# Performance work log

Hardware: AMD Instinct MI355X
Metric: run time of the kernel (lower is better)

## Reference

```python
import jax, jax.numpy as jnp
import numpy as np
from jax import lax

T_H = 16
B = 16384
GW, GH = 3, 13          # masks are (B, grid_w, grid_h, enc) so permute -> (B, enc, 13, 3)
ENC = 64                # encoder_size
IN_EMB = 32             # input_embedding_size
DYN = 32                # dyn_embedding_size
SCD = 64                # soc_conv_depth
C31 = 16                # conv_3x1_depth
SOC_EMB = ((GH - 4 + 1) // 2) * C31  # 80
N_CELLS = B * GW * GH
N_NBRS = (N_CELLS + 1) // 2  # every other grid cell occupied -> 319488
NEG_SLOPE = 0.1


def leaky(x):
    return jnp.where(x >= 0, x, NEG_SLOPE * x)


def lstm_last_hidden(x, Wih, Whh, bih, bhh):
    """x: (T, N, in). PyTorch gate order i,f,g,o. Returns final h: (N, H)."""
    H = Whh.shape[1]
    N = x.shape[1]
    b = bih + bhh
    def step(carry, xt):
        h, c = carry
        gates = xt @ Wih.T + h @ Whh.T + b  # (N, 4H)
        i, f, g, o = jnp.split(gates, 4, axis=-1)
        c = jax.nn.sigmoid(f) * c + jax.nn.sigmoid(i) * jnp.tanh(g)
        h = jax.nn.sigmoid(o) * jnp.tanh(c)
        return (h, c), None
    h0 = jnp.zeros((N, H), x.dtype)
    (h, _), _ = lax.scan(step, (h0, h0), x)
    return h


def conv2d(x, W, b, ):
    y = lax.conv_general_dilated(x, W, window_strides=(1, 1), padding='VALID',
                                 dimension_numbers=('NCHW', 'OIHW', 'NCHW'))
    return y + b[None, :, None, None]


def setup_inputs() -> dict:
    key = jax.random.key(0)
    ks = jax.random.split(key, 10)
    hist = jax.random.normal(ks[0], (T_H, B, 2), jnp.float32)
    nbrs = jax.random.normal(ks[1], (T_H, N_NBRS, 2), jnp.float32)
    # Occupancy: every other cell; masked_scatter_ fills a full 64-vector per occupied cell.
    flat_occ = (jnp.arange(N_CELLS) % 2) == 0
    masks = jnp.broadcast_to(flat_occ.reshape(B, GW, GH, 1), (B, GW, GH, ENC))
    s = 0.05
    W_ip = jax.random.normal(ks[2], (IN_EMB, 2), jnp.float32) * s
    b_ip = jnp.zeros((IN_EMB,), jnp.float32)
    Wih = jax.random.normal(ks[3], (4 * ENC, IN_EMB), jnp.float32) * s
    Whh = jax.random.normal(ks[4], (4 * ENC, ENC), jnp.float32) * s
    bih = jnp.zeros((4 * ENC,), jnp.float32)
    bhh = jnp.zeros((4 * ENC,), jnp.float32)
    W_dyn = jax.random.normal(ks[5], (DYN, ENC), jnp.float32) * s
    b_dyn = jnp.zeros((DYN,), jnp.float32)
    W_sc = jax.random.normal(ks[6], (SCD, ENC, 3, 3), jnp.float32) * s
    b_sc = jnp.zeros((SCD,), jnp.float32)
    W_c31 = jax.random.normal(ks[7], (C31, SCD, 3, 1), jnp.float32) * s
    b_c31 = jnp.zeros((C31,), jnp.float32)
    return dict(hist=hist, nbrs=nbrs, masks=masks, W_ip=W_ip, b_ip=b_ip,
                Wih=Wih, Whh=Whh, bih=bih, bhh=bhh, W_dyn=W_dyn, b_dyn=b_dyn,
                W_sc=W_sc, b_sc=b_sc, W_c31=W_c31, b_c31=b_c31)


def reference(hist, nbrs, masks, W_ip, b_ip, Wih, Whh, bih, bhh,
              W_dyn, b_dyn, W_sc, b_sc, W_c31, b_c31):
    # 1. ego dynamics
    hist_emb = leaky(hist @ W_ip.T + b_ip)                 # (T, B, 32)
    hist_enc = lstm_last_hidden(hist_emb, Wih, Whh, bih, bhh)  # (B, 64)
    hist_enc = leaky(hist_enc @ W_dyn.T + b_dyn)           # (B, 32)
    # 2. neighbour encodings
    nbrs_emb = leaky(nbrs @ W_ip.T + b_ip)                 # (T, N, 32)
    nbrs_enc = lstm_last_hidden(nbrs_emb, Wih, Whh, bih, bhh)  # (N, 64)
    # 3. masked_scatter_: scatter nbrs_enc rows into occupied grid cells in row-major order
    occ = masks[:, :, :, 0].reshape(-1)                    # (B*GW*GH,) bool
    idx = jnp.cumsum(occ.astype(jnp.int32)) - 1            # nbr index per occupied cell
    gathered = nbrs_enc[jnp.clip(idx, 0, None)]            # (B*GW*GH, 64)
    soc = jnp.where(occ[:, None], gathered, 0.0).reshape(B, GW, GH, ENC)
    # 4. permute(0,3,2,1) -> (B, enc, GH, GW)
    soc = soc.transpose(0, 3, 2, 1)
    soc = leaky(conv2d(soc, W_sc, b_sc))                   # (B, 64, 11, 1)
    soc = leaky(conv2d(soc, W_c31, b_c31))                 # (B, 16, 9, 1)
    # 5. MaxPool2d((2,1), padding=(1,0)) with -inf padding
    soc = lax.reduce_window(soc, -jnp.inf, lax.max,
                            window_dimensions=(1, 1, 2, 1), window_strides=(1, 1, 2, 1),
                            padding=((0, 0), (0, 0), (1, 1), (0, 0)))  # (B,16,5,1)
    soc = soc.reshape(-1, SOC_EMB)                         # (B, 80)
    return jnp.concatenate([soc, hist_enc], axis=1)        # (B, 112)
```

## Files before the change

kernel.cpp:

```cpp
#include <hip/hip_runtime.h>
#include <cstdint>

#define T_H 16
#define B_SZ 16384
#define NN 319488

#define EROWP 40
#define HROWP 72
#define W1R 72
#define NB_NBR 4992
#define NB_HIST 256
#define CHUNK 8192
#define O1STR 704
#define LOG2E 1.4426950408889634f
#define M2L   2.8853900817779268f

typedef __attribute__((ext_vector_type(8))) _Float16 f16x8;
typedef __attribute__((ext_vector_type(4))) float f32x4;

__device__ __forceinline__ float lrelu(float x) { return fmaxf(x, 0.1f * x); }

__device__ __forceinline__ f16x8 cvt8(const float* __restrict__ p, float sc) {
    float4 a = ((const float4*)p)[0];
    float4 b = ((const float4*)p)[1];
    f16x8 r;
    r[0] = (_Float16)(a.x * sc); r[1] = (_Float16)(a.y * sc);
    r[2] = (_Float16)(a.z * sc); r[3] = (_Float16)(a.w * sc);
    r[4] = (_Float16)(b.x * sc); r[5] = (_Float16)(b.y * sc);
    r[6] = (_Float16)(b.z * sc); r[7] = (_Float16)(b.w * sc);
    return r;
}

__global__ __launch_bounds__(256, 3) void lstm_coop(
    const float* __restrict__ hist, const float* __restrict__ nbrs,
    const float* __restrict__ Wip, const float* __restrict__ bip,
    const float* __restrict__ Wih, const float* __restrict__ Whh,
    const float* __restrict__ bsum,
    const float* __restrict__ Wdyn, const float* __restrict__ bdyn,
    _Float16* __restrict__ ench, float* __restrict__ out)
{
    __shared__ alignas(16) _Float16 eb[2][64 * EROWP];
    __shared__ alignas(16) _Float16 hb[2][64 * HROWP];

    const int tid = threadIdx.x;
    const int wid = tid >> 6;
    const int lane = tid & 63;
    const int col = lane & 15;
    const int quad = lane >> 4;

    const bool ishist = (blockIdx.x >= NB_NBR);
    const int seq0 = (ishist ? (blockIdx.x - NB_NBR) : blockIdx.x) * 64;
    const int N = ishist ? B_SZ : NN;
    const float2* __restrict__ xp = (const float2*)(ishist ? hist : nbrs);

    f16x8 Bv[4][3];
#pragma unroll
    for (int gt = 0; gt < 4; gt++) {
        const float sc = (gt == 2) ? M2L : -LOG2E;
        const int row = gt * 64 + wid * 16 + col;
        Bv[gt][0] = cvt8(Wih + row * 32 + quad * 8,      sc);
        Bv[gt][1] = cvt8(Whh + row * 64 + quad * 8,      sc);
        Bv[gt][2] = cvt8(Whh + row * 64 + 32 + quad * 8, sc);
    }
    float bg4[4];
#pragma unroll
    for (int gt = 0; gt < 4; gt++) bg4[gt] = bsum[gt * 64 + wid * 16 + col];

    float wipx[8], wipy[8], bipv[8];
#pragma unroll
    for (int u = 0; u < 8; u++) {
        int j = quad * 8 + u;
        wipx[u] = Wip[2 * j]; wipy[u] = Wip[2 * j + 1]; bipv[u] = bip[j];
    }

    float c[16];
#pragma unroll
    for (int q = 0; q < 16; q++) c[q] = 0.0f;

    {
        float2 xv = xp[seq0 + wid * 16 + col];
        f16x8 E;
#pragma unroll
        for (int u = 0; u < 8; u++)
            E[u] = (_Float16)lrelu(fmaf(xv.x, wipx[u], fmaf(xv.y, wipy[u], bipv[u])));
        *(f16x8*)&eb[0][(wid * 16 + col) * EROWP + quad * 8] = E;
    }
    __syncthreads();

#pragma unroll 1
    for (int t = 0; t < T_H; t++) {
        const int cur = t & 1;
        float2 xn{0.f, 0.f};
        if (t < T_H - 1) xn = xp[(size_t)(t + 1) * N + seq0 + wid * 16 + col];

#pragma unroll
        for (int s = 0; s < 4; s++) {
            const int er = (s * 16 + col) * EROWP + quad * 8;
            f16x8 ehv = *(const f16x8*)&eb[cur][er];
            f32x4 acc[4];
#pragma unroll
            for (int gt = 0; gt < 4; gt++)
                acc[gt] = f32x4{bg4[gt], bg4[gt], bg4[gt], bg4[gt]};
#pragma unroll
            for (int gt = 0; gt < 4; gt++)
                acc[gt] = __builtin_amdgcn_mfma_f32_16x16x32_f16(ehv, Bv[gt][0], acc[gt], 0, 0, 0);
            if (t) {
                const int hr = (s * 16 + col) * HROWP + quad * 8;
                f16x8 h0 = *(const f16x8*)&hb[cur ^ 1][hr];
                f16x8 h1 = *(const f16x8*)&hb[cur ^ 1][hr + 32];
#pragma unroll
                for (int gt = 0; gt < 4; gt++) {
                    acc[gt] = __builtin_amdgcn_mfma_f32_16x16x32_f16(h0, Bv[gt][1], acc[gt], 0, 0, 0);
                    acc[gt] = __builtin_amdgcn_mfma_f32_16x16x32_f16(h1, Bv[gt][2], acc[gt], 0, 0, 0);
                }
            }
#pragma unroll
            for (int r = 0; r < 4; r++) {
                float ei = __builtin_amdgcn_exp2f(acc[0][r]);
                float ef = __builtin_amdgcn_exp2f(acc[1][r]);
                float eg = __builtin_amdgcn_exp2f(acc[2][r]);
                float pf = 1.0f + ef;
                float P  = (1.0f + ei) * (1.0f + eg);
                float cc = fmaf(eg - 1.0f, pf, c[s * 4 + r] * P)
                         * __builtin_amdgcn_rcpf(pf * P);
                c[s * 4 + r] = cc;
                float eo = __builtin_amdgcn_exp2f(acc[3][r]);
                float ec = __builtin_amdgcn_exp2f(M2L * cc);
                float h = (ec - 1.0f) * __builtin_amdgcn_rcpf((1.0f + eo) * (1.0f + ec));
                hb[cur][(s * 16 + quad * 4 + r) * HROWP + wid * 16 + col] = (_Float16)h;
            }
        }

        if (t < T_H - 1) {
            f16x8 E;
#pragma unroll
            for (int u = 0; u < 8; u++)
                E[u] = (_Float16)lrelu(fmaf(xn.x, wipx[u], fmaf(xn.y, wipy[u], bipv[u])));
            *(f16x8*)&eb[cur ^ 1][(wid * 16 + col) * EROWP + quad * 8] = E;
        }
        __syncthreads();
    }

    if (!ishist) {
#pragma unroll 1
        for (int r = 0; r < 16; r++) {
            int sl = wid * 16 + r;
            ench[(size_t)(seq0 + sl) * 64 + lane] = hb[1][sl * HROWP + lane];
        }
    } else {
        float a2[8];
#pragma unroll
        for (int u = 0; u < 8; u++) a2[u] = bdyn[quad * 8 + u];
        const int hr = (wid * 16 + col) * HROWP;
#pragma unroll 1
        for (int j = 0; j < 64; j++) {
            float hv = (float)hb[1][hr + j];
#pragma unroll
            for (int u = 0; u < 8; u++)
                a2[u] = fmaf(hv, Wdyn[(quad * 8 + u) * 64 + j], a2[u]);
        }
#pragma unroll
        for (int u = 0; u < 8; u++)
            out[(size_t)(seq0 + wid * 16 + col) * 112 + 80 + quad * 8 + u] = lrelu(a2[u]);
    }
}

__global__ void prep(const float* __restrict__ Wsc, const float* __restrict__ Wc31,
                     const float* __restrict__ bih, const float* __restrict__ bhh,
                     _Float16* __restrict__ wq_g, float* __restrict__ w2t,
                     float* __restrict__ bsum)
{
    int t = blockIdx.x * 256 + threadIdx.x;
    if (t < 9 * 64 * W1R) {
        int tap = t / (64 * W1R), rem = t - tap * (64 * W1R);
        int oc = rem / W1R, ch = rem - oc * W1R;
        float w = (ch < 64) ? Wsc[oc * 576 + ch * 9 + tap] : 0.0f;
        wq_g[t] = (_Float16)w;
    }
    if (t < 3072) { int oc = t / 192, r = t - oc * 192; w2t[r * 16 + oc] = Wc31[t]; }
    if (t < 256) {
        float sc = ((t >> 6) == 2) ? M2L : -LOG2E;
        bsum[t] = (bih[t] + bhh[t]) * sc;
    }
}

__global__ __launch_bounds__(128, 1) void conv1_mfma(
    const _Float16* __restrict__ ench, const _Float16* __restrict__ wq_g,
    const float* __restrict__ bsc, float* __restrict__ o1, int bchunk0)
{
    __shared__ alignas(16) _Float16 wq[9 * 64 * W1R];
    const int tid = threadIdx.x;
    for (int i = tid; i < 9 * 64 * W1R / 8; i += 128)
        ((uint4*)wq)[i] = ((const uint4*)wq_g)[i];
    __syncthreads();

    const int cls = tid >> 6;
    const int lane = tid & 63;
    const int col = lane & 15, quad = lane >> 4;
    const int b0 = bchunk0 + blockIdx.x * 32;
    const int bA = b0 + 2 * col + cls;

    float bn[4];
#pragma unroll
    for (int n = 0; n < 4; n++) bn[n] = bsc[n * 16 + col];

#pragma unroll 1
    for (int y = 0; y < 11; y++) {
        f32x4 ac[4];
#pragma unroll
        for (int n = 0; n < 4; n++) ac[n] = f32x4{bn[n], bn[n], bn[n], bn[n]};
        const int P = (cls + y) & 1;
#pragma unroll
        for (int tap = 0; tap < 9; tap++) {
            const int dy = tap / 3, dx = tap - dy * 3;
            if (((dy + dx) & 1) != P) continue;
            const int row = (bA * 39 + dx * 13 + y + dy) >> 1;
#pragma unroll
            for (int kt = 0; kt < 2; kt++) {
                const size_t ao = (size_t)row * 64 + kt * 32 + quad * 8;
                f16x8 Ah = *(const f16x8*)(ench + ao);
#pragma unroll
                for (int n = 0; n < 4; n++) {
                    f16x8 Bh = *(const f16x8*)&wq[(tap * 64 + n * 16 + col) * W1R + kt * 32 + quad * 8];
                    ac[n] = __builtin_amdgcn_mfma_f32_16x16x32_f16(Ah, Bh, ac[n], 0, 0, 0);
                }
            }
        }
        const int bOb = blockIdx.x * 32 + cls;
#pragma unroll
        for (int r = 0; r < 4; r++) {
            const int bO = bOb + 2 * (quad * 4 + r);
#pragma unroll
            for (int n = 0; n < 4; n++)
                o1[(size_t)bO * O1STR + y * 64 + n * 16 + col] = lrelu(ac[n][r]);
        }
    }
}

__global__ __launch_bounds__(256, 2) void conv2_pool(
    const float* __restrict__ o1, const float* __restrict__ w2t,
    const float* __restrict__ bc31, float* __restrict__ out, int bchunk0)
{
    __shared__ float tile[16 * 772];
    __shared__ float w2s[3072];
    const int t = threadIdx.x;
    const int bl0 = blockIdx.x * 16;
    for (int i = t; i < 3072; i += 256) w2s[i] = w2t[i];
    for (int u = t; u < 16 * 176; u += 256) {
        int b = u / 176, r = u - b * 176;
        float4 v = ((const float4*)(o1 + (size_t)(bl0 + b) * O1STR))[r];
        int y = r >> 4, i = (r & 15) << 2;
        float* dst = tile + b * 772 + i * 12 + y;
        dst[0] = v.x; dst[12] = v.y; dst[24] = v.z; dst[36] = v.w;
    }
    __syncthreads();

    const int b = t & 15, oc2 = t >> 4;
    float acc[9];
#pragma unroll
    for (int y2 = 0; y2 < 9; y2++) acc[y2] = bc31[oc2];
    const float* tb = tile + b * 772;
#pragma unroll 2
    for (int i = 0; i < 64; i++) {
        const float* rowp = tb + i * 12;
        float4 p0 = *(const float4*)(rowp);
        float4 p1 = *(const float4*)(rowp + 4);
        float4 p2 = *(const float4*)(rowp + 8);
        float w0 = w2s[i * 48 + oc2];
        float w1 = w2s[i * 48 + 16 + oc2];
        float w2 = w2s[i * 48 + 32 + oc2];
        float a[12] = {p0.x, p0.y, p0.z, p0.w, p1.x, p1.y, p1.z, p1.w, p2.x, p2.y, p2.z, p2.w};
#pragma unroll
        for (int y2 = 0; y2 < 9; y2++)
            acc[y2] = fmaf(a[y2], w0, fmaf(a[y2 + 1], w1, fmaf(a[y2 + 2], w2, acc[y2])));
    }
    float* op = out + (size_t)(bchunk0 + bl0 + b) * 112 + oc2 * 5;
    op[0] = lrelu(acc[0]);
#pragma unroll
    for (int y5 = 1; y5 < 5; y5++)
        op[y5] = lrelu(fmaxf(acc[2 * y5 - 1], acc[2 * y5]));
}

extern "C" void kernel_launch(void* const* d_in, const int* in_sizes, int n_in,
                              void* d_out, int out_size, void* d_ws, size_t ws_size,
                              hipStream_t stream)
{
    const float* hist = (const float*)d_in[0];
    const float* nbrs = (const float*)d_in[1];
    const float* Wip  = (const float*)d_in[3];
    const float* bip  = (const float*)d_in[4];
    const float* Wih  = (const float*)d_in[5];
    const float* Whh  = (const float*)d_in[6];
    const float* bih  = (const float*)d_in[7];
    const float* bhh  = (const float*)d_in[8];
    const float* Wdyn = (const float*)d_in[9];
    const float* bdyn = (const float*)d_in[10];
    const float* Wsc  = (const float*)d_in[11];
    const float* bsc  = (const float*)d_in[12];
    const float* Wc31 = (const float*)d_in[13];
    const float* bc31 = (const float*)d_in[14];
    float* out = (float*)d_out;

    _Float16* ench = (_Float16*)d_ws;
    _Float16* wq_g = ench + (size_t)NN * 64;
    float*    w2t  = (float*)(wq_g + 9 * 64 * W1R);
    float*    bsum = w2t + 3072;
    float*    o1   = bsum + 256;

    prep<<<162, 256, 0, stream>>>(Wsc, Wc31, bih, bhh, wq_g, w2t, bsum);
    lstm_coop<<<NB_NBR + NB_HIST, 256, 0, stream>>>(hist, nbrs, Wip, bip, Wih, Whh,
                                                    bsum, Wdyn, bdyn, ench, out);
    for (int ch = 0; ch < 2; ch++) {
        conv1_mfma<<<CHUNK / 32, 128, 0, stream>>>(ench, wq_g, bsc, o1, ch * CHUNK);
        conv2_pool<<<CHUNK / 16, 256, 0, stream>>>(o1, w2t, bc31, out, ch * CHUNK);
    }
}
```

Baseline: 720.2 us.

## Swizzle conv1 weight LDS layout, unchunk conv launches, raise LSTM occupancy

Result: slower. 2.248 ms (+212.1%).

```diff
diff --git a/kernel.cpp b/kernel.cpp
--- a/kernel.cpp
+++ b/kernel.cpp
@@ -7,10 +7,8 @@
 
 #define EROWP 40
 #define HROWP 72
-#define W1R 72
 #define NB_NBR 4992
 #define NB_HIST 256
-#define CHUNK 8192
 #define O1STR 704
 #define LOG2E 1.4426950408889634f
 #define M2L   2.8853900817779268f
@@ -31,7 +29,7 @@
     return r;
 }
 
-__global__ __launch_bounds__(256, 3) void lstm_coop(
+__global__ __launch_bounds__(256, 5) void lstm_coop(
     const float* __restrict__ hist, const float* __restrict__ nbrs,
     const float* __restrict__ Wip, const float* __restrict__ bip,
     const float* __restrict__ Wih, const float* __restrict__ Whh,
@@ -171,11 +169,11 @@
                      float* __restrict__ bsum)
 {
     int t = blockIdx.x * 256 + threadIdx.x;
-    if (t < 9 * 64 * W1R) {
-        int tap = t / (64 * W1R), rem = t - tap * (64 * W1R);
-        int oc = rem / W1R, ch = rem - oc * W1R;
-        float w = (ch < 64) ? Wsc[oc * 576 + ch * 9 + tap] : 0.0f;
-        wq_g[t] = (_Float16)w;
+    if (t < 9 * 64 * 64) {
+        int tap = t >> 12, rem = t & 4095;
+        int oc = rem >> 6, o = rem & 63;
+        int ch = ((((o >> 3) ^ (oc & 7)) << 3) | (o & 7));
+        wq_g[t] = (_Float16)Wsc[oc * 576 + ch * 9 + tap];
     }
     if (t < 3072) { int oc = t / 192, r = t - oc * 192; w2t[r * 16 + oc] = Wc31[t]; }
     if (t < 256) {
@@ -186,18 +184,18 @@
 
 __global__ __launch_bounds__(128, 1) void conv1_mfma(
     const _Float16* __restrict__ ench, const _Float16* __restrict__ wq_g,
-    const float* __restrict__ bsc, float* __restrict__ o1, int bchunk0)
-{
-    __shared__ alignas(16) _Float16 wq[9 * 64 * W1R];
+    const float* __restrict__ bsc, float* __restrict__ o1)
+{
+    __shared__ alignas(16) _Float16 wq[9 * 64 * 64];
     const int tid = threadIdx.x;
-    for (int i = tid; i < 9 * 64 * W1R / 8; i += 128)
+    for (int i = tid; i < 9 * 64 * 64 / 8; i += 128)
         ((uint4*)wq)[i] = ((const uint4*)wq_g)[i];
     __syncthreads();
 
     const int cls = tid >> 6;
     const int lane = tid & 63;
     const int col = lane & 15, quad = lane >> 4;
-    const int b0 = bchunk0 + blockIdx.x * 32;
+    const int b0 = blockIdx.x * 32;
     const int bA = b0 + 2 * col + cls;
 
     float bn[4];
@@ -221,15 +219,15 @@
                 f16x8 Ah = *(const f16x8*)(ench + ao);
 #pragma unroll
                 for (int n = 0; n < 4; n++) {
-                    f16x8 Bh = *(const f16x8*)&wq[(tap * 64 + n * 16 + col) * W1R + kt * 32 + quad * 8];
+                    f16x8 Bh = *(const f16x8*)&wq[((tap * 64 + n * 16 + col) << 6)
+                                                  + ((((kt << 2) + quad) ^ (col & 7)) << 3)];
                     ac[n] = __builtin_amdgcn_mfma_f32_16x16x32_f16(Ah, Bh, ac[n], 0, 0, 0);
                 }
             }
         }
-        const int bOb = blockIdx.x * 32 + cls;
 #pragma unroll
         for (int r = 0; r < 4; r++) {
-            const int bO = bOb + 2 * (quad * 4 + r);
+            const int bO = b0 + cls + 2 * (quad * 4 + r);
 #pragma unroll
             for (int n = 0; n < 4; n++)
                 o1[(size_t)bO * O1STR + y * 64 + n * 16 + col] = lrelu(ac[n][r]);
@@ -239,7 +237,7 @@
 
 __global__ __launch_bounds__(256, 2) void conv2_pool(
     const float* __restrict__ o1, const float* __restrict__ w2t,
-    const float* __restrict__ bc31, float* __restrict__ out, int bchunk0)
+    const float* __restrict__ bc31, float* __restrict__ out)
 {
     __shared__ float tile[16 * 772];
     __shared__ float w2s[3072];
@@ -274,7 +272,7 @@
         for (int y2 = 0; y2 < 9; y2++)
             acc[y2] = fmaf(a[y2], w0, fmaf(a[y2 + 1], w1, fmaf(a[y2 + 2], w2, acc[y2])));
     }
-    float* op = out + (size_t)(bchunk0 + bl0 + b) * 112 + oc2 * 5;
+    float* op = out + (size_t)(bl0 + b) * 112 + oc2 * 5;
     op[0] = lrelu(acc[0]);
 #pragma unroll
     for (int y5 = 1; y5 < 5; y5++)
@@ -303,15 +301,13 @@
 
     _Float16* ench = (_Float16*)d_ws;
     _Float16* wq_g = ench + (size_t)NN * 64;
-    float*    w2t  = (float*)(wq_g + 9 * 64 * W1R);
+    float*    w2t  = (float*)(wq_g + 9 * 64 * 64);
     float*    bsum = w2t + 3072;
     float*    o1   = bsum + 256;
 
-    prep<<<162, 256, 0, stream>>>(Wsc, Wc31, bih, bhh, wq_g, w2t, bsum);
+    prep<<<144, 256, 0, stream>>>(Wsc, Wc31, bih, bhh, wq_g, w2t, bsum);
     lstm_coop<<<NB_NBR + NB_HIST, 256, 0, stream>>>(hist, nbrs, Wip, bip, Wih, Whh,
                                                     bsum, Wdyn, bdyn, ench, out);
-    for (int ch = 0; ch < 2; ch++) {
-        conv1_mfma<<<CHUNK / 32, 128, 0, stream>>>(ench, wq_g, bsc, o1, ch * CHUNK);
-        conv2_pool<<<CHUNK / 16, 256, 0, stream>>>(o1, w2t, bc31, out, ch * CHUNK);
-    }
-}
+    conv1_mfma<<<512, 128, 0, stream>>>(ench, wq_g, bsc, o1);
+    conv2_pool<<<1024, 256, 0, stream>>>(o1, w2t, bc31, out);
+}
```
